# Kernel tuning notes

Measured on AMD Instinct MI355X. Metric: run time of the kernel, lower is better.

Reference implementation:

```python
import jax, jax.numpy as jnp
import numpy as np

B, C, H, W, D = 512, 256, 6, 8, 8


def setup_inputs() -> dict:
    key = jax.random.key(0)
    k1, k2, k3 = jax.random.split(key, 3)
    x = jax.random.normal(k1, (B, C, H, W, D), dtype=jnp.float32)
    adj = jax.random.normal(k2, (C, C), dtype=jnp.float32)
    para = jax.random.normal(k3, (1, C, H, W, D), dtype=jnp.float32)
    return {"x": x, "adj": adj, "para": para}


def reference(x, adj, para):
    b, c, h, w, d = x.shape
    fea = x.reshape(b, c, h * w * d)              # (b, c, HWD)
    c_adj = x.mean(axis=(2, 3, 4))                # AdaptiveAvgPool3d(1) -> (b, c)
    # torch: t1 (1,c), t2 (c,1); (t1 - t2)[i, j] = c_adj[j] - c_adj[i]
    diff = c_adj[:, None, :] - c_adj[:, :, None]  # (b, c, c)
    s = jnp.abs(jnp.abs(jax.nn.sigmoid(diff) - 0.5) - 0.5) * 2.0
    s = (s + jnp.swapaxes(s, 1, 2)) * 0.5         # symmetrize
    # batched (adj * s) @ fea  -> (b, c, HWD)
    out = jnp.einsum('bij,bjk->bik', adj[None, :, :] * s, fea)
    out = out.reshape(b, c, h, w, d) * para       # broadcast (1,c,h,w,d)
    return jax.nn.relu(out)
```

## Files before the change

kernel.cpp:

```cpp
#include <hip/hip_runtime.h>

#define B_   512
#define C_   256
#define HWD_ 384

typedef __bf16 bf16x8 __attribute__((ext_vector_type(8)));
typedef float  f32x4  __attribute__((ext_vector_type(4)));

#define CSWZ(r) (((r) ^ ((r) >> 2)) & 3)

__global__ __launch_bounds__(256) void mean_kernel(const float* __restrict__ x,
                                                   float* __restrict__ cadj) {
    const int row  = (blockIdx.x << 2) + (threadIdx.x >> 6);
    const int lane = threadIdx.x & 63;
    const float2* p = (const float2*)(x + (size_t)row * HWD_);
    float s = 0.f;
#pragma unroll
    for (int t = 0; t < 3; ++t) {
        float2 v = p[lane + (t << 6)];
        s += v.x + v.y;
    }
#pragma unroll
    for (int off = 32; off; off >>= 1) s += __shfl_xor(s, off, 64);
    if (lane == 0) cadj[row] = s * (1.0f / HWD_);
}

__global__ __launch_bounds__(512) void gemm_fused(const float* __restrict__ x,
                                                  const float* __restrict__ adj,
                                                  const float* __restrict__ para,
                                                  const float* __restrict__ cadj,
                                                  float* __restrict__ out) {
    const int nt = blockIdx.x;
    const int b  = blockIdx.y;
    const int n0 = nt * 128;

    __shared__ __bf16 As[256 * 32];
    __shared__ __bf16 Bs[128 * 32];
    __shared__ float  ca_s[C_];

    const int t    = threadIdx.x;
    const int lane = t & 63;
    const int w    = t >> 6;
    const int wm   = w & 3;
    const int wn   = w >> 2;
    const int lm   = lane & 15, quad = lane >> 4;

    if (t < C_) ca_s[t] = cadj[b * C_ + t];
    __syncthreads();

    const int ai = t >> 1, ah = t & 1;
    const float ca_i = ca_s[ai];
    const float* aglob = adj + (size_t)ai * C_ + ah * 16;
    char* arow = (char*)As + (size_t)ai * 64;
    const int asw = CSWZ(ai);
    char* adst0 = arow + (((2 * ah)     ^ asw) << 4);
    char* adst1 = arow + (((2 * ah + 1) ^ asw) << 4);

    const int kq8 = t >> 7, bn = t & 127;
    const float* bglob = x + (size_t)(b * C_ + 8 * kq8) * HWD_ + n0 + bn;
    char* bdst = (char*)Bs + (size_t)bn * 64 + ((kq8 ^ CSWZ(bn)) << 4);

    const char* afp[4];
    const char* bfp[4];
#pragma unroll
    for (int mm = 0; mm < 4; ++mm) {
        const int ra = wm * 64 + mm * 16 + lm;
        afp[mm] = (const char*)As + (size_t)ra * 64 + ((quad ^ CSWZ(ra)) << 4);
    }
#pragma unroll
    for (int nn = 0; nn < 4; ++nn) {
        const int rb = wn * 64 + nn * 16 + lm;
        bfp[nn] = (const char*)Bs + (size_t)rb * 64 + ((quad ^ CSWZ(rb)) << 4);
    }

    f32x4 acc[4][4];
#pragma unroll
    for (int mm = 0; mm < 4; ++mm)
#pragma unroll
        for (int nn = 0; nn < 4; ++nn)
            acc[mm][nn] = (f32x4){0.f, 0.f, 0.f, 0.f};

    for (int k0 = 0; k0 < C_; k0 += 32) {
        __syncthreads();
        {
            const float* ap = aglob + k0;
            float4 av[4];
#pragma unroll
            for (int q = 0; q < 4; ++q) av[q] = ((const float4*)ap)[q];
            bf16x8 pk0, pk1;
#pragma unroll
            for (int jj = 0; jj < 16; ++jj) {
                float aval = ((const float*)av)[jj];
                float d  = ca_s[k0 + ah * 16 + jj] - ca_i;
                float tt = __expf(-fabsf(d));
                float s  = 2.f * tt / (1.f + tt);
                float v  = aval * s;
                if (jj < 8) pk0[jj & 7] = (__bf16)v;
                else        pk1[jj & 7] = (__bf16)v;
            }
            *(bf16x8*)adst0 = pk0;
            *(bf16x8*)adst1 = pk1;
        }
        {
            float f[8];
#pragma unroll
            for (int j = 0; j < 8; ++j)
                f[j] = bglob[(size_t)(k0 + j) * HWD_];
            bf16x8 pk;
#pragma unroll
            for (int j = 0; j < 8; ++j) pk[j] = (__bf16)f[j];
            *(bf16x8*)bdst = pk;
        }
        __syncthreads();
        bf16x8 af[4], bfr[4];
#pragma unroll
        for (int mm = 0; mm < 4; ++mm) af[mm]  = *(const bf16x8*)afp[mm];
#pragma unroll
        for (int nn = 0; nn < 4; ++nn) bfr[nn] = *(const bf16x8*)bfp[nn];
#pragma unroll
        for (int mm = 0; mm < 4; ++mm)
#pragma unroll
            for (int nn = 0; nn < 4; ++nn)
                acc[mm][nn] = __builtin_amdgcn_mfma_f32_16x16x32_bf16(
                    af[mm], bfr[nn], acc[mm][nn], 0, 0, 0);
    }

#pragma unroll
    for (int mm = 0; mm < 4; ++mm) {
#pragma unroll
        for (int r = 0; r < 4; ++r) {
            const int i = wm * 64 + mm * 16 + quad * 4 + r;
            const float* pp = para + (size_t)i * HWD_ + n0;
            float* op = out + ((size_t)b * C_ + i) * HWD_ + n0;
#pragma unroll
            for (int nn = 0; nn < 4; ++nn) {
                const int n = wn * 64 + nn * 16 + lm;
                float v = acc[mm][nn][r] * pp[n];
                op[n] = v > 0.f ? v : 0.f;
            }
        }
    }
}

extern "C" void kernel_launch(void* const* d_in, const int* in_sizes, int n_in,
                              void* d_out, int out_size, void* d_ws, size_t ws_size,
                              hipStream_t stream) {
    const float* x    = (const float*)d_in[0];
    const float* adj  = (const float*)d_in[1];
    const float* para = (const float*)d_in[2];
    float* out  = (float*)d_out;
    float* cadj = (float*)d_ws;

    mean_kernel<<<dim3((B_ * C_) / 4), 256, 0, stream>>>(x, cadj);
    gemm_fused<<<dim3(3, B_), 512, 0, stream>>>(x, adj, para, cadj, out);
}
```

Before: 454.6 us.

## Prefetch next K-slice into registers and raise MFMA wave priority

Software-pipelines the GEMM K loop by loading the next adj and x slices into registers before processing the current slice, so global load latency overlaps the sigmoid math and MFMA work. The loop is fully unrolled and the LDS barrier moves to the end of each iteration. It also uses a hardware reciprocal in place of the division and wraps the MFMA block in s_setprio. The cost is higher register pressure from the prefetch buffers, which could reduce occupancy at 512 threads per block.

Result: faster. 404.2 us (-11.1%).

```diff
diff --git a/kernel.cpp b/kernel.cpp
--- a/kernel.cpp
+++ b/kernel.cpp
@@ -46,10 +46,8 @@
     const int lm   = lane & 15, quad = lane >> 4;
 
     if (t < C_) ca_s[t] = cadj[b * C_ + t];
-    __syncthreads();
 
     const int ai = t >> 1, ah = t & 1;
-    const float ca_i = ca_s[ai];
     const float* aglob = adj + (size_t)ai * C_ + ah * 16;
     char* arow = (char*)As + (size_t)ai * 64;
     const int asw = CSWZ(ai);
@@ -73,6 +71,16 @@
         bfp[nn] = (const char*)Bs + (size_t)rb * 64 + ((quad ^ CSWZ(rb)) << 4);
     }
 
+    __syncthreads();
+    const float ca_i = ca_s[ai];
+
+    float4 avc[4];
+    float  fbc[8];
+#pragma unroll
+    for (int q = 0; q < 4; ++q) avc[q] = ((const float4*)aglob)[q];
+#pragma unroll
+    for (int j = 0; j < 8; ++j)  fbc[j] = bglob[(size_t)j * HWD_];
+
     f32x4 acc[4][4];
 #pragma unroll
     for (int mm = 0; mm < 4; ++mm)
@@ -80,49 +88,64 @@
         for (int nn = 0; nn < 4; ++nn)
             acc[mm][nn] = (f32x4){0.f, 0.f, 0.f, 0.f};
 
-    for (int k0 = 0; k0 < C_; k0 += 32) {
-        __syncthreads();
+#pragma unroll
+    for (int s = 0; s < 8; ++s) {
+        const int k0 = s * 32;
+
+        float4 avn[4];
+        float  fbn[8];
+        if (s < 7) {
+#pragma unroll
+            for (int q = 0; q < 4; ++q)
+                avn[q] = ((const float4*)(aglob + k0 + 32))[q];
+#pragma unroll
+            for (int j = 0; j < 8; ++j)
+                fbn[j] = bglob[(size_t)(k0 + 32 + j) * HWD_];
+        }
+
+        bf16x8 pk0, pk1;
         {
-            const float* ap = aglob + k0;
-            float4 av[4];
-#pragma unroll
-            for (int q = 0; q < 4; ++q) av[q] = ((const float4*)ap)[q];
-            bf16x8 pk0, pk1;
+            const float* cah = &ca_s[k0 + ah * 16];
 #pragma unroll
             for (int jj = 0; jj < 16; ++jj) {
-                float aval = ((const float*)av)[jj];
-                float d  = ca_s[k0 + ah * 16 + jj] - ca_i;
+                float aval = ((const float*)avc)[jj];
+                float d  = cah[jj] - ca_i;
                 float tt = __expf(-fabsf(d));
-                float s  = 2.f * tt / (1.f + tt);
-                float v  = aval * s;
+                float sg = 2.f * tt * __builtin_amdgcn_rcpf(1.f + tt);
+                float v  = aval * sg;
                 if (jj < 8) pk0[jj & 7] = (__bf16)v;
                 else        pk1[jj & 7] = (__bf16)v;
             }
-            *(bf16x8*)adst0 = pk0;
-            *(bf16x8*)adst1 = pk1;
         }
-        {
-            float f[8];
+        bf16x8 pkB;
 #pragma unroll
-            for (int j = 0; j < 8; ++j)
-                f[j] = bglob[(size_t)(k0 + j) * HWD_];
-            bf16x8 pk;
-#pragma unroll
-            for (int j = 0; j < 8; ++j) pk[j] = (__bf16)f[j];
-            *(bf16x8*)bdst = pk;
-        }
+        for (int j = 0; j < 8; ++j) pkB[j] = (__bf16)fbc[j];
+        *(bf16x8*)adst0 = pk0;
+        *(bf16x8*)adst1 = pk1;
+        *(bf16x8*)bdst  = pkB;
         __syncthreads();
+
         bf16x8 af[4], bfr[4];
 #pragma unroll
         for (int mm = 0; mm < 4; ++mm) af[mm]  = *(const bf16x8*)afp[mm];
 #pragma unroll
         for (int nn = 0; nn < 4; ++nn) bfr[nn] = *(const bf16x8*)bfp[nn];
+        __builtin_amdgcn_s_setprio(1);
 #pragma unroll
         for (int mm = 0; mm < 4; ++mm)
 #pragma unroll
             for (int nn = 0; nn < 4; ++nn)
                 acc[mm][nn] = __builtin_amdgcn_mfma_f32_16x16x32_bf16(
                     af[mm], bfr[nn], acc[mm][nn], 0, 0, 0);
+        __builtin_amdgcn_s_setprio(0);
+        __syncthreads();
+
+        if (s < 7) {
+#pragma unroll
+            for (int q = 0; q < 4; ++q) avc[q] = avn[q];
+#pragma unroll
+            for (int j = 0; j < 8; ++j)  fbc[j] = fbn[j];
+        }
     }
 
 #pragma unroll
```
